# Optimization experiments

Measured on AMD Instinct MI355X. Metric: run time of the kernel, lower is better.

## Reference

```python
import jax, jax.numpy as jnp
import numpy as np

O, NI, F, D, NN, M = 2048, 16, 4, 128, 8, 8  # outfits, item slots, factors, dim, neighbors, valid slots
D2 = D // 2

def lrelu(x):
    return jax.nn.leaky_relu(x, 0.01)

def mlp2(x, W1, b1, W2, b2):
    # Linear -> LeakyReLU -> Linear -> LeakyReLU (Dropout is identity at inference)
    return lrelu(lrelu(x @ W1 + b1) @ W2 + b2)

def setup_inputs():
    ks = jax.random.split(jax.random.key(0), 16)
    s = 0.05
    pos = jnp.arange(NI)[None, :]
    outfit_items = jnp.where(pos < M, jax.random.randint(ks[0], (O, NI), 0, NI), -1)
    items_neighbor = jax.random.randint(ks[1], (O, NI, NN), -1, NI)
    items_feature = jax.random.normal(ks[2], (O, NI, D), dtype=jnp.float32)
    items_factors = jnp.zeros((O, NI, F, D), dtype=jnp.float32)
    p = {
        'cf_W1': jax.random.normal(ks[3], (F, D, D2)) * s,
        'cf_b1': jnp.zeros((F, D2)),
        'cf_W2': jax.random.normal(ks[4], (F, D2, D)) * s,
        'cf_b2': jnp.zeros((F, D)),
        'f2f_W1': jax.random.normal(ks[5], (D, D)) * s, 'f2f_b1': jnp.zeros((D,)),
        'f2f_W2': jax.random.normal(ks[6], (D, D)) * s, 'f2f_b2': jnp.zeros((D,)),
        'f2i_W1': jax.random.normal(ks[7], (D, D)) * s, 'f2i_b1': jnp.zeros((D,)),
        'f2i_W2': jax.random.normal(ks[8], (D, D)) * s, 'f2i_b2': jnp.zeros((D,)),
        'i2i_W1': jax.random.normal(ks[9], (D, D)) * s, 'i2i_b1': jnp.zeros((D,)),
        'i2i_W2': jax.random.normal(ks[10], (D, D)) * s, 'i2i_b2': jnp.zeros((D,)),
        'o2s_W': jax.random.normal(ks[11], (D, 1)) * s, 'o2s_b': jnp.zeros((1,)),
    }
    return dict(outfit_items=outfit_items, items_feature=items_feature,
                items_neighbor=items_neighbor, items_factors=items_factors, **p)

def _forward(outfit_items, items_feature, items_neighbor, items_factors,
             cf_W1, cf_b1, cf_W2, cf_b2, f2f_W1, f2f_b1, f2f_W2, f2f_b2,
             f2i_W1, f2i_b1, f2i_W2, f2i_b2, i2i_W1, i2i_b1, i2i_W2, i2i_b2,
             o2s_W, o2s_b):
    del items_factors  # creat_factors overwrites every entry in the original
    # --- creat_factors: per-factor 2-layer MLP on every item feature -> [O,NI,F,D]
    h = lrelu(jnp.einsum('oid,fde->oife', items_feature, cf_W1) + cf_b1)
    fac = lrelu(jnp.einsum('oife,fed->oifd', h, cf_W2) + cf_b2)

    # --- inter_factors: sequential over outfit slots; later slots read updated factors
    def outfit_fac(fac_o, oi_o, nbr_o):
        def step(f, i):
            valid = i != -1
            ic = jnp.maximum(i, 0)
            cand = jnp.concatenate([oi_o, nbr_o[ic]])                # [NI+NN]
            cm = (cand != -1) & (cand != i) & valid
            t = f[ic]                                                # [F,D] snapshot
            msg = mlp2(t[None] * f[jnp.maximum(cand, 0)],
                       f2f_W1, f2f_b1, f2f_W2, f2f_b2)               # [NI+NN,F,D]
            add = jnp.sum(jnp.where(cm[:, None, None], msg, 0.0), axis=0)
            return f.at[ic].add(jnp.where(valid, add, 0.0)), None
        f, _ = jax.lax.scan(step, fac_o, oi_o)
        return f
    fac = jax.vmap(outfit_fac)(fac, outfit_items, items_neighbor)

    # --- infer_items: feature[i] += sum_j f2i(fac[i,j]) for outfit members
    g = mlp2(fac, f2i_W1, f2i_b1, f2i_W2, f2i_b2).sum(axis=2)        # [O,NI,D]
    ic = jnp.maximum(outfit_items, 0)
    w = (outfit_items != -1).astype(g.dtype)                          # [O,NI]
    gsel = jnp.take_along_axis(g, ic[..., None], axis=1)
    scat = jax.vmap(lambda gs, idx, ww: jnp.zeros((NI, D), gs.dtype).at[idx].add(ww[:, None] * gs))
    feat = items_feature + scat(gsel, ic, w)

    # --- inter_items: sequential; current value detached (.data in original)
    def outfit_feat(fo_init, oi_o):
        jc = jnp.maximum(oi_o, 0)
        def step(fo, i):
            valid = i != -1
            ic_ = jnp.maximum(i, 0)
            t = jax.lax.stop_gradient(fo[ic_])
            msgs = mlp2(fo[jc], i2i_W1, i2i_b1, i2i_W2, i2i_b2)      # [NI,D]
            m = ((oi_o != -1) & (oi_o != i)).astype(fo.dtype)
            new = t + jnp.sum(m[:, None] * msgs, axis=0)
            return jnp.where(valid, fo.at[ic_].set(new), fo), None
        fo, _ = jax.lax.scan(step, fo_init, oi_o)
        return fo
    feat = jax.vmap(outfit_feat)(feat, outfit_items)

    # --- infer_outfit + score
    fsel = jnp.take_along_axis(feat, ic[..., None], axis=1)
    outfits = jnp.sum(w[..., None] * fsel, axis=1)                    # [O,D]
    scores = jax.nn.sigmoid(outfits @ o2s_W + o2s_b)[:, 0]            # [O]

    # --- com_loss: ||F F^T - I||_F^2 over valid slots (positional mask), / n_outfits
    G = jnp.einsum('oifd,oigd->oifg', fac, fac) - jnp.eye(F, dtype=fac.dtype)
    com = jnp.sum(w * jnp.sum(G * G, axis=(-1, -2))) / O
    return scores, jnp.reshape(com, (1,))

def reference(outfit_items, items_feature, items_neighbor, items_factors,
              cf_W1, cf_b1, cf_W2, cf_b2, f2f_W1, f2f_b1, f2f_W2, f2f_b2,
              f2i_W1, f2i_b1, f2i_W2, f2i_b2, i2i_W1, i2i_b1, i2i_W2, i2i_b2,
              o2s_W, o2s_b):
    return _forward(outfit_items, items_feature, items_neighbor, items_factors,
                    cf_W1, cf_b1, cf_W2, cf_b2, f2f_W1, f2f_b1, f2f_W2, f2f_b2,
                    f2i_W1, f2i_b1, f2i_W2, f2i_b2, i2i_W1, i2i_b1, i2i_W2, i2i_b2,
                    o2s_W, o2s_b)
```

## Files before the change

kernel.cpp:

```cpp
#include <hip/hip_runtime.h>
#include <hip/hip_bf16.h>
#include <math.h>


typedef __attribute__((ext_vector_type(8))) short short8;
typedef __attribute__((ext_vector_type(4))) float f32x4;

#define MFMA16(a, b, c) __builtin_amdgcn_mfma_f32_16x16x32_bf16(a, b, c, 0, 0, 0)

__device__ __forceinline__ float lrelu(float x) { return fmaxf(x, 0.01f * x); }

__device__ __forceinline__ ushort f2bf(float f) {
  unsigned u = __builtin_bit_cast(unsigned, f);
  u += 0x7fffu + ((u >> 16) & 1u);
  return (ushort)(u >> 16);
}
__device__ __forceinline__ float bflo(unsigned u) {
  return __builtin_bit_cast(float, u << 16);
}
__device__ __forceinline__ unsigned pk2(float a, float b) {
  float2 t; t.x = a; t.y = b;
  __hip_bfloat162 h = __float22bfloat162_rn(t);
  unsigned u;
  __builtin_memcpy(&u, &h, 4);
  return u;
}


__global__ __launch_bounds__(256) void prep_weights(
    const float* __restrict__ cfW1, const float* __restrict__ cfW2,
    const float* __restrict__ f2fW1, const float* __restrict__ f2fW2,
    const float* __restrict__ f2iW1, const float* __restrict__ f2iW2,
    const float* __restrict__ i2iW1, const float* __restrict__ i2iW2,
    ushort* __restrict__ ws, float* __restrict__ out) {
  const int idx = (int)(blockIdx.x * 256 + threadIdx.x);
  if (idx == 0) out[2048] = 0.0f;
  float v;
  if (idx < 32768) {
    int f = idx >> 13, r = idx & 8191, n = r >> 7, k = r & 127;
    v = cfW1[f * 8192 + k * 64 + n];
  } else if (idx < 65536) {
    int t = idx - 32768;
    int f = t >> 13, r = t & 8191, n = r >> 6, k = r & 63;
    v = cfW2[f * 8192 + k * 128 + n];
  } else {
    int t = idx - 65536;
    int seg = t >> 14, r = t & 16383, n = r >> 7, k = r & 127;
    const float* W = (seg == 0) ? f2fW1 : (seg == 1) ? f2fW2 :
                     (seg == 2) ? f2iW1 : (seg == 3) ? f2iW2 :
                     (seg == 4) ? i2iW1 : i2iW2;
    v = W[k * 128 + n];
  }
  ws[idx] = f2bf(v);
}

__global__ __launch_bounds__(512, 2) void mfgn_kernel(
    const int* __restrict__ outfit_items,
    const float* __restrict__ items_feature,
    const int* __restrict__ items_neighbor,
    const float* __restrict__ cfb1, const float* __restrict__ cfb2,
    const float* __restrict__ f2fb1, const float* __restrict__ f2fb2,
    const float* __restrict__ f2ib1, const float* __restrict__ f2ib2,
    const float* __restrict__ i2ib1, const float* __restrict__ i2ib2,
    const float* __restrict__ o2sW, const float* __restrict__ o2sb,
    const ushort* __restrict__ wsW,
    float* __restrict__ out)
{
  __shared__ float facL[16 * 528];
  __shared__ ushort prodS[64 * 136] __attribute__((aligned(16)));
  __shared__ ushort hidS[64 * 136] __attribute__((aligned(16)));
  __shared__ ushort featB[16 * 136] __attribute__((aligned(16)));
  __shared__ float redE[8];
  __shared__ int oiL[16];
  __shared__ int clAll[256];
  __shared__ int ncAll[16];
  __shared__ int vslL[16];
  __shared__ int refcntL[16];
  __shared__ int nvsL;

  const int o = blockIdx.x;
  const int tid = (int)threadIdx.x;
  const int lane = tid & 63;
  const int wid = tid >> 6;
  const int n16 = lane & 15;
  const int q = lane >> 4;
  const int kb = q * 8;
  const int col = wid * 16 + n16;
  const int fS = lane & 3, ciS = lane >> 2;
  const int kc0 = wid * 16;

  if (tid < 16) oiL[tid] = outfit_items[o * 16 + tid];
  {
    const int n = tid >> 5, d0 = (tid & 31) * 4;
    float4 v = *(const float4*)(items_feature + o * 2048 + tid * 4);
    uint2 pk; pk.x = pk2(v.x, v.y); pk.y = pk2(v.z, v.w);
    *(uint2*)(featB + n * 136 + d0) = pk;
  }
  if (tid == 0) {
    int cnt = 0;
    for (int s = 0; s < 16; ++s) refcntL[s] = 0;
    for (int s = 0; s < 16; ++s) {
      int v = oiL[s];
      if (v != -1) { vslL[cnt++] = s; refcntL[v]++; }
    }
    nvsL = cnt;
  }
  for (int s = wid; s < 16; s += 8) {
    const int iv = outfit_items[o * 16 + s];
    if (iv == -1) { if (lane == 0) ncAll[s] = 0; continue; }
    int cand = -1;
    if (lane < 24) cand = (lane < 16) ? outfit_items[o * 16 + lane]
                                      : items_neighbor[o * 128 + iv * 8 + (lane - 16)];
    bool ok = (lane < 24) && (cand != -1) && (cand != iv);
    unsigned long long bm = __ballot(ok);
    if (ok) clAll[s * 16 + __popcll(bm & ((1ull << lane) - 1ull))] = cand;
    if (lane == 0) ncAll[s] = (int)__popcll(bm);
  }
  __syncthreads();
  const int nvs = nvsL;

  {
    const int f = wid & 3, half = wid >> 2;
    short8 wA[2][4];
#pragma unroll
    for (int etl = 0; etl < 2; ++etl)
#pragma unroll
      for (int kt = 0; kt < 4; ++kt)
        wA[etl][kt] = *(const short8*)(wsW + (f * 64 + (half * 2 + etl) * 16 + n16) * 128
                                       + kt * 32 + kb);
    f32x4 acc[2];
#pragma unroll
    for (int etl = 0; etl < 2; ++etl)
      acc[etl] = *(const f32x4*)(cfb1 + f * 64 + (half * 2 + etl) * 16 + q * 4);
    for (int kt = 0; kt < 4; ++kt) {
      short8 x = *(const short8*)(featB + n16 * 136 + kt * 32 + kb);
      acc[0] = MFMA16(wA[0][kt], x, acc[0]);
      acc[1] = MFMA16(wA[1][kt], x, acc[1]);
    }
#pragma unroll
    for (int etl = 0; etl < 2; ++etl) {
      float h0 = lrelu(acc[etl][0]), h1 = lrelu(acc[etl][1]);
      float h2 = lrelu(acc[etl][2]), h3 = lrelu(acc[etl][3]);
      uint2 pk; pk.x = pk2(h0, h1); pk.y = pk2(h2, h3);
      *(uint2*)(hidS + (f * 16 + n16) * 136 + (half * 2 + etl) * 16 + q * 4) = pk;
    }
    __syncthreads();
    short8 wB[4][2];
#pragma unroll
    for (int ctl = 0; ctl < 4; ++ctl)
#pragma unroll
      for (int kt = 0; kt < 2; ++kt)
        wB[ctl][kt] = *(const short8*)(wsW + 32768 + (f * 128 + half * 64 + ctl * 16 + n16) * 64
                                       + kt * 32 + kb);
    f32x4 acc2[4];
#pragma unroll
    for (int ctl = 0; ctl < 4; ++ctl) {
      float b2 = cfb2[f * 128 + half * 64 + ctl * 16 + n16];
      acc2[ctl] = (f32x4){b2, b2, b2, b2};
    }
    for (int kt = 0; kt < 2; ++kt) {
      short8 h = *(const short8*)(hidS + (f * 16 + n16) * 136 + kt * 32 + kb);
#pragma unroll
      for (int ctl = 0; ctl < 4; ++ctl) acc2[ctl] = MFMA16(h, wB[ctl][kt], acc2[ctl]);
    }
#pragma unroll
    for (int ctl = 0; ctl < 4; ++ctl) {
      int c = half * 64 + ctl * 16 + n16;
#pragma unroll
      for (int r = 0; r < 4; ++r)
        facL[(q * 4 + r) * 528 + f * 132 + c] = lrelu(acc2[ctl][r]);
    }
    __syncthreads();
  }

  {
    short8 w1f[4], w2f[4];
#pragma unroll
    for (int kt = 0; kt < 4; ++kt) {
      w1f[kt] = *(const short8*)(wsW + 65536 + col * 128 + kt * 32 + kb);
      w2f[kt] = *(const short8*)(wsW + 81920 + col * 128 + kt * 32 + kb);
    }
    const f32x4 b1q = *(const f32x4*)(f2fb1 + wid * 16 + q * 4);
    const float b2v = f2fb2[col];

    auto stageB = [&](int s, int iv_, int nc_) {
      if (ciS < nc_) {
        const int cit = clAll[s * 16 + ciS];
        const float* tp = facL + iv_ * 528 + fS * 132 + kc0;
        const float* cp = facL + cit * 528 + fS * 132 + kc0;
#pragma unroll
        for (int i2 = 0; i2 < 2; ++i2) {
          float4 a0 = *(const float4*)(tp + i2 * 8), a1 = *(const float4*)(tp + i2 * 8 + 4);
          float4 c0 = *(const float4*)(cp + i2 * 8), c1 = *(const float4*)(cp + i2 * 8 + 4);
          uint4 u4;
          u4.x = pk2(a0.x * c0.x, a0.y * c0.y); u4.y = pk2(a0.z * c0.z, a0.w * c0.w);
          u4.z = pk2(a1.x * c1.x, a1.y * c1.y); u4.w = pk2(a1.z * c1.z, a1.w * c1.w);
          *(uint4*)(prodS + lane * 136 + kc0 + i2 * 8) = u4;
        }
      }
    };
    auto stageC = [&]() {
      const float* sp = facL + ciS * 528 + fS * 132 + kc0;
#pragma unroll
      for (int i2 = 0; i2 < 2; ++i2) {
        float4 a0 = *(const float4*)(sp + i2 * 8), a1 = *(const float4*)(sp + i2 * 8 + 4);
        uint4 u4;
        u4.x = pk2(a0.x, a0.y); u4.y = pk2(a0.z, a0.w);
        u4.z = pk2(a1.x, a1.y); u4.w = pk2(a1.z, a1.w);
        *(uint4*)(prodS + lane * 136 + kc0 + i2 * 8) = u4;
      }
    };

    if (nvs > 0) { const int s0 = vslL[0]; stageB(s0, oiL[s0], ncAll[s0]); }
    __syncthreads();

    for (int u = 0; u < nvs; ++u) {
      const int s = vslL[u];
      const int iv = oiL[s];
      const int nc = ncAll[s];
      f32x4 acc[4];
#pragma unroll
      for (int mt = 0; mt < 4; ++mt) acc[mt] = b1q;
      for (int kt = 0; kt < 4; ++kt)
#pragma unroll
        for (int mt = 0; mt < 4; ++mt) {
          short8 x = *(const short8*)(prodS + (mt * 16 + n16) * 136 + kt * 32 + kb);
          acc[mt] = MFMA16(w1f[kt], x, acc[mt]);
        }
#pragma unroll
      for (int mt = 0; mt < 4; ++mt) {
        float h0 = lrelu(acc[mt][0]), h1 = lrelu(acc[mt][1]);
        float h2 = lrelu(acc[mt][2]), h3 = lrelu(acc[mt][3]);
        uint2 pk; pk.x = pk2(h0, h1); pk.y = pk2(h2, h3);
        *(uint2*)(hidS + (mt * 16 + n16) * 136 + wid * 16 + q * 4) = pk;
      }
      __syncthreads();
      f32x4 acc2[4];
#pragma unroll
      for (int mt = 0; mt < 4; ++mt) acc2[mt] = (f32x4){b2v, b2v, b2v, b2v};
      for (int kt = 0; kt < 4; ++kt)
#pragma unroll
        for (int mt = 0; mt < 4; ++mt) {
          short8 h = *(const short8*)(hidS + (mt * 16 + n16) * 136 + kt * 32 + kb);
          acc2[mt] = MFMA16(h, w2f[kt], acc2[mt]);
        }
      float part[4] = {0.f, 0.f, 0.f, 0.f};
#pragma unroll
      for (int mt = 0; mt < 4; ++mt) {
        bool act = (mt * 4 + q) < nc;
        if (act) {
#pragma unroll
          for (int r = 0; r < 4; ++r) part[r] += lrelu(acc2[mt][r]);
        }
      }
#pragma unroll
      for (int r = 0; r < 4; ++r) {
        float v = part[r];
        v += __shfl_xor(v, 16);
        v += __shfl_xor(v, 32);
        part[r] = v;
      }
      if (q == 0) {
#pragma unroll
        for (int r = 0; r < 4; ++r)
          facL[iv * 528 + r * 132 + col] += part[r];
      }
      if (u + 1 < nvs) {
        const int s2 = vslL[u + 1];
        stageB(s2, oiL[s2], ncAll[s2]);
      } else {
        stageC();
      }
      __syncthreads();
    }
    if (nvs == 0) { stageC(); __syncthreads(); }
  }

  {
    short8 w1f[4], w2f[4];
#pragma unroll
    for (int kt = 0; kt < 4; ++kt) {
      w1f[kt] = *(const short8*)(wsW + 98304 + col * 128 + kt * 32 + kb);
      w2f[kt] = *(const short8*)(wsW + 114688 + col * 128 + kt * 32 + kb);
    }
    const f32x4 b1q = *(const f32x4*)(f2ib1 + wid * 16 + q * 4);
    const float b2v = f2ib2[col];
    f32x4 acc[4];
#pragma unroll
    for (int mt = 0; mt < 4; ++mt) acc[mt] = b1q;
    for (int kt = 0; kt < 4; ++kt)
#pragma unroll
      for (int mt = 0; mt < 4; ++mt) {
        short8 x = *(const short8*)(prodS + (mt * 16 + n16) * 136 + kt * 32 + kb);
        acc[mt] = MFMA16(w1f[kt], x, acc[mt]);
      }
#pragma unroll
    for (int mt = 0; mt < 4; ++mt) {
      float h0 = lrelu(acc[mt][0]), h1 = lrelu(acc[mt][1]);
      float h2 = lrelu(acc[mt][2]), h3 = lrelu(acc[mt][3]);
      uint2 pk; pk.x = pk2(h0, h1); pk.y = pk2(h2, h3);
      *(uint2*)(hidS + (mt * 16 + n16) * 136 + wid * 16 + q * 4) = pk;
    }
    __syncthreads();
    f32x4 acc2[4];
#pragma unroll
    for (int mt = 0; mt < 4; ++mt) acc2[mt] = (f32x4){b2v, b2v, b2v, b2v};
    for (int kt = 0; kt < 4; ++kt)
#pragma unroll
      for (int mt = 0; mt < 4; ++mt) {
        short8 h = *(const short8*)(hidS + (mt * 16 + n16) * 136 + kt * 32 + kb);
        acc2[mt] = MFMA16(h, w2f[kt], acc2[mt]);
      }
#pragma unroll
    for (int mt = 0; mt < 4; ++mt) {
      int item = mt * 4 + q;
      float g = 0.f;
#pragma unroll
      for (int r = 0; r < 4; ++r) g += lrelu(acc2[mt][r]);
      int a = item * 136 + col;
      featB[a] = f2bf(bflo((unsigned)featB[a]) + (float)refcntL[item] * g);
    }
    __syncthreads();
  }

  {
    short8 w1f[4], w2f[4];
#pragma unroll
    for (int kt = 0; kt < 4; ++kt) {
      w1f[kt] = *(const short8*)(wsW + 131072 + col * 128 + kt * 32 + kb);
      w2f[kt] = *(const short8*)(wsW + 147456 + col * 128 + kt * 32 + kb);
    }
    const f32x4 b1q = *(const f32x4*)(i2ib1 + wid * 16 + q * 4);
    const float b2v = i2ib2[col];
    short8 xc[4];
#pragma unroll
    for (int kt = 0; kt < 4; ++kt)
      xc[kt] = *(const short8*)(featB + n16 * 136 + kt * 32 + kb);

    for (int u = 0; u < nvs; ++u) {
      const int iv = oiL[vslL[u]];
      f32x4 acc = b1q;
      for (int kt = 0; kt < 4; ++kt) acc = MFMA16(w1f[kt], xc[kt], acc);
      {
        float h0 = lrelu(acc[0]), h1 = lrelu(acc[1]);
        float h2 = lrelu(acc[2]), h3 = lrelu(acc[3]);
        uint2 pk; pk.x = pk2(h0, h1); pk.y = pk2(h2, h3);
        *(uint2*)(hidS + n16 * 136 + wid * 16 + q * 4) = pk;
      }
      __syncthreads();
      f32x4 acc2 = (f32x4){b2v, b2v, b2v, b2v};
      for (int kt = 0; kt < 4; ++kt) {
        short8 h = *(const short8*)(hidS + n16 * 136 + kt * 32 + kb);
        acc2 = MFMA16(h, w2f[kt], acc2);
      }
      float part = 0.f;
#pragma unroll
      for (int r = 0; r < 4; ++r) {
        int item = q * 4 + r;
        float w = (item == iv) ? 0.0f : (float)refcntL[item];
        part += w * lrelu(acc2[r]);
      }
      part += __shfl_xor(part, 16);
      part += __shfl_xor(part, 32);
      if (q == 0) {
        int a = iv * 136 + col;
        featB[a] = f2bf(bflo((unsigned)featB[a]) + part);
      }
      __syncthreads();
      if (n16 == iv) {
#pragma unroll
        for (int kt = 0; kt < 4; ++kt)
          xc[kt] = *(const short8*)(featB + n16 * 136 + kt * 32 + kb);
      }
    }
  }

  if (tid < 128) {
    float sum = 0.0f;
    for (int u = 0; u < nvs; ++u)
      sum += bflo((unsigned)featB[oiL[vslL[u]] * 136 + tid]);
    float v = sum * o2sW[tid];
#pragma unroll
    for (int off = 1; off < 64; off <<= 1) v += __shfl_xor(v, off);
    if (lane == 0) redE[wid] = v;
  }
  __syncthreads();
  if (tid == 0) {
    float t = redE[0] + redE[1] + o2sb[0];
    out[o] = 1.0f / (1.0f + expf(-t));
  }

  {
    const int n = tid >> 5, f = (tid >> 3) & 3, g = (tid >> 1) & 3, h = tid & 1;
    float dot = 0.0f;
    if (f <= g) {
      const float* pa = facL + n * 528 + f * 132 + h * 64;
      const float* pb = facL + n * 528 + g * 132 + h * 64;
      for (int i = 0; i < 16; ++i) {
        float4 a = *(const float4*)(pa + i * 4);
        float4 b = *(const float4*)(pb + i * 4);
        dot += a.x * b.x + a.y * b.y + a.z * b.z + a.w * b.w;
      }
    }
    dot += __shfl_xor(dot, 1);
    float v = dot - ((f == g) ? 1.0f : 0.0f);
    float wgt = (f == g) ? 1.0f : 2.0f;
    float sq = (h == 0 && f <= g && oiL[n] != -1) ? wgt * v * v : 0.0f;
#pragma unroll
    for (int off = 1; off < 64; off <<= 1) sq += __shfl_xor(sq, off);
    __syncthreads();
    if (lane == 0) redE[wid] = sq;
    __syncthreads();
    if (tid == 0) {
      float tot = 0.f;
#pragma unroll
      for (int w = 0; w < 8; ++w) tot += redE[w];
      atomicAdd(out + 2048, tot * (1.0f / 2048.0f));
    }
  }
}

extern "C" void kernel_launch(void* const* d_in, const int* in_sizes, int n_in,
                              void* d_out, int out_size, void* d_ws, size_t ws_size,
                              hipStream_t stream) {
  float* out = (float*)d_out;
  ushort* ws = (ushort*)d_ws;
  hipLaunchKernelGGL(prep_weights, dim3(640), dim3(256), 0, stream,
                     (const float*)d_in[4], (const float*)d_in[6],
                     (const float*)d_in[8], (const float*)d_in[10],
                     (const float*)d_in[12], (const float*)d_in[14],
                     (const float*)d_in[16], (const float*)d_in[18],
                     ws, out);
  hipLaunchKernelGGL(mfgn_kernel, dim3(2048), dim3(512), 0, stream,
                     (const int*)d_in[0],
                     (const float*)d_in[1],
                     (const int*)d_in[2],
                     (const float*)d_in[5], (const float*)d_in[7],
                     (const float*)d_in[9], (const float*)d_in[11],
                     (const float*)d_in[13], (const float*)d_in[15],
                     (const float*)d_in[17], (const float*)d_in[19],
                     (const float*)d_in[20], (const float*)d_in[21],
                     (const ushort*)ws,
                     out);
}
```

Before: 336.5 us.

## Store MFMA operand tiles in lane-contiguous fragment layout in shared memory

Replaces the padded row-major (stride 136) shared-memory layouts of prodS, hidS and featB with a fragment-ordered layout. Each MFMA B-operand read becomes a contiguous lane*8 short8 load at a tile base, and writers compute swizzled addresses instead. This aims to cut LDS bank conflicts and address arithmetic in the inner MFMA loops, at the cost of more complex and scattered store and element-access indexing.

```diff
diff --git a/kernel.cpp b/kernel.cpp
--- a/kernel.cpp
+++ b/kernel.cpp
@@ -67,9 +67,9 @@
     float* __restrict__ out)
 {
   __shared__ float facL[16 * 528];
-  __shared__ ushort prodS[64 * 136] __attribute__((aligned(16)));
-  __shared__ ushort hidS[64 * 136] __attribute__((aligned(16)));
-  __shared__ ushort featB[16 * 136] __attribute__((aligned(16)));
+  __shared__ ushort prodS[8192] __attribute__((aligned(16)));
+  __shared__ ushort hidS[8192] __attribute__((aligned(16)));
+  __shared__ ushort featB[2048] __attribute__((aligned(16)));
   __shared__ float redE[8];
   __shared__ int oiL[16];
   __shared__ int clAll[256];
@@ -86,15 +86,20 @@
   const int q = lane >> 4;
   const int kb = q * 8;
   const int col = wid * 16 + n16;
+  const int lx = lane * 8;
   const int fS = lane & 3, ciS = lane >> 2;
   const int kc0 = wid * 16;
+  const int q0 = (wid & 1) * 2;
+  const int sWA = ((wid >> 1) * 4 + (lane >> 4)) * 512 + (lane & 15) * 8;
+  const int hwB = (wid >> 1) * 2048 + ((wid & 1) * 2 + (q >> 1)) * 128 + n16 * 8 + (q & 1) * 4;
+  const int fbCol = (col >> 5) * 512 + ((col >> 3) & 3) * 128 + (col & 7);
 
   if (tid < 16) oiL[tid] = outfit_items[o * 16 + tid];
   {
     const int n = tid >> 5, d0 = (tid & 31) * 4;
     float4 v = *(const float4*)(items_feature + o * 2048 + tid * 4);
     uint2 pk; pk.x = pk2(v.x, v.y); pk.y = pk2(v.z, v.w);
-    *(uint2*)(featB + n * 136 + d0) = pk;
+    *(uint2*)(featB + (d0 >> 5) * 512 + (((d0 >> 3) & 3) * 16 + n) * 8 + (d0 & 7)) = pk;
   }
   if (tid == 0) {
     int cnt = 0;
@@ -133,7 +138,7 @@
     for (int etl = 0; etl < 2; ++etl)
       acc[etl] = *(const f32x4*)(cfb1 + f * 64 + (half * 2 + etl) * 16 + q * 4);
     for (int kt = 0; kt < 4; ++kt) {
-      short8 x = *(const short8*)(featB + n16 * 136 + kt * 32 + kb);
+      short8 x = *(const short8*)(featB + kt * 512 + lx);
       acc[0] = MFMA16(wA[0][kt], x, acc[0]);
       acc[1] = MFMA16(wA[1][kt], x, acc[1]);
     }
@@ -142,7 +147,8 @@
       float h0 = lrelu(acc[etl][0]), h1 = lrelu(acc[etl][1]);
       float h2 = lrelu(acc[etl][2]), h3 = lrelu(acc[etl][3]);
       uint2 pk; pk.x = pk2(h0, h1); pk.y = pk2(h2, h3);
-      *(uint2*)(hidS + (f * 16 + n16) * 136 + (half * 2 + etl) * 16 + q * 4) = pk;
+      *(uint2*)(hidS + half * 2048 + f * 512 + (etl * 2 + (q >> 1)) * 128
+                + n16 * 8 + (q & 1) * 4) = pk;
     }
     __syncthreads();
     short8 wB[4][2];
@@ -159,7 +165,7 @@
       acc2[ctl] = (f32x4){b2, b2, b2, b2};
     }
     for (int kt = 0; kt < 2; ++kt) {
-      short8 h = *(const short8*)(hidS + (f * 16 + n16) * 136 + kt * 32 + kb);
+      short8 h = *(const short8*)(hidS + (kt * 4 + f) * 512 + lx);
 #pragma unroll
       for (int ctl = 0; ctl < 4; ++ctl) acc2[ctl] = MFMA16(h, wB[ctl][kt], acc2[ctl]);
     }
@@ -189,25 +195,25 @@
         const float* tp = facL + iv_ * 528 + fS * 132 + kc0;
         const float* cp = facL + cit * 528 + fS * 132 + kc0;
 #pragma unroll
-        for (int i2 = 0; i2 < 2; ++i2) {
-          float4 a0 = *(const float4*)(tp + i2 * 8), a1 = *(const float4*)(tp + i2 * 8 + 4);
-          float4 c0 = *(const float4*)(cp + i2 * 8), c1 = *(const float4*)(cp + i2 * 8 + 4);
+        for (int g = 0; g < 2; ++g) {
+          float4 a0 = *(const float4*)(tp + g * 8), a1 = *(const float4*)(tp + g * 8 + 4);
+          float4 c0 = *(const float4*)(cp + g * 8), c1 = *(const float4*)(cp + g * 8 + 4);
           uint4 u4;
           u4.x = pk2(a0.x * c0.x, a0.y * c0.y); u4.y = pk2(a0.z * c0.z, a0.w * c0.w);
           u4.z = pk2(a1.x * c1.x, a1.y * c1.y); u4.w = pk2(a1.z * c1.z, a1.w * c1.w);
-          *(uint4*)(prodS + lane * 136 + kc0 + i2 * 8) = u4;
+          *(uint4*)(prodS + sWA + (q0 + g) * 128) = u4;
         }
       }
     };
     auto stageC = [&]() {
       const float* sp = facL + ciS * 528 + fS * 132 + kc0;
 #pragma unroll
-      for (int i2 = 0; i2 < 2; ++i2) {
-        float4 a0 = *(const float4*)(sp + i2 * 8), a1 = *(const float4*)(sp + i2 * 8 + 4);
+      for (int g = 0; g < 2; ++g) {
+        float4 a0 = *(const float4*)(sp + g * 8), a1 = *(const float4*)(sp + g * 8 + 4);
         uint4 u4;
         u4.x = pk2(a0.x, a0.y); u4.y = pk2(a0.z, a0.w);
         u4.z = pk2(a1.x, a1.y); u4.w = pk2(a1.z, a1.w);
-        *(uint4*)(prodS + lane * 136 + kc0 + i2 * 8) = u4;
+        *(uint4*)(prodS + sWA + (q0 + g) * 128) = u4;
       }
     };
 
@@ -224,7 +230,7 @@
       for (int kt = 0; kt < 4; ++kt)
 #pragma unroll
         for (int mt = 0; mt < 4; ++mt) {
-          short8 x = *(const short8*)(prodS + (mt * 16 + n16) * 136 + kt * 32 + kb);
+          short8 x = *(const short8*)(prodS + (kt * 4 + mt) * 512 + lx);
           acc[mt] = MFMA16(w1f[kt], x, acc[mt]);
         }
 #pragma unroll
@@ -232,7 +238,7 @@
         float h0 = lrelu(acc[mt][0]), h1 = lrelu(acc[mt][1]);
         float h2 = lrelu(acc[mt][2]), h3 = lrelu(acc[mt][3]);
         uint2 pk; pk.x = pk2(h0, h1); pk.y = pk2(h2, h3);
-        *(uint2*)(hidS + (mt * 16 + n16) * 136 + wid * 16 + q * 4) = pk;
+        *(uint2*)(hidS + hwB + mt * 512) = pk;
       }
       __syncthreads();
       f32x4 acc2[4];
@@ -241,7 +247,7 @@
       for (int kt = 0; kt < 4; ++kt)
 #pragma unroll
         for (int mt = 0; mt < 4; ++mt) {
-          short8 h = *(const short8*)(hidS + (mt * 16 + n16) * 136 + kt * 32 + kb);
+          short8 h = *(const short8*)(hidS + (kt * 4 + mt) * 512 + lx);
           acc2[mt] = MFMA16(h, w2f[kt], acc2[mt]);
         }
       float part[4] = {0.f, 0.f, 0.f, 0.f};
@@ -291,7 +297,7 @@
     for (int kt = 0; kt < 4; ++kt)
 #pragma unroll
       for (int mt = 0; mt < 4; ++mt) {
-        short8 x = *(const short8*)(prodS + (mt * 16 + n16) * 136 + kt * 32 + kb);
+        short8 x = *(const short8*)(prodS + (kt * 4 + mt) * 512 + lx);
         acc[mt] = MFMA16(w1f[kt], x, acc[mt]);
       }
 #pragma unroll
@@ -299,7 +305,7 @@
       float h0 = lrelu(acc[mt][0]), h1 = lrelu(acc[mt][1]);
       float h2 = lrelu(acc[mt][2]), h3 = lrelu(acc[mt][3]);
       uint2 pk; pk.x = pk2(h0, h1); pk.y = pk2(h2, h3);
-      *(uint2*)(hidS + (mt * 16 + n16) * 136 + wid * 16 + q * 4) = pk;
+      *(uint2*)(hidS + hwB + mt * 512) = pk;
     }
     __syncthreads();
     f32x4 acc2[4];
@@ -308,7 +314,7 @@
     for (int kt = 0; kt < 4; ++kt)
 #pragma unroll
       for (int mt = 0; mt < 4; ++mt) {
-        short8 h = *(const short8*)(hidS + (mt * 16 + n16) * 136 + kt * 32 + kb);
+        short8 h = *(const short8*)(hidS + (kt * 4 + mt) * 512 + lx);
         acc2[mt] = MFMA16(h, w2f[kt], acc2[mt]);
       }
 #pragma unroll
@@ -317,7 +323,7 @@
       float g = 0.f;
 #pragma unroll
       for (int r = 0; r < 4; ++r) g += lrelu(acc2[mt][r]);
-      int a = item * 136 + col;
+      int a = fbCol + item * 8;
       featB[a] = f2bf(bflo((unsigned)featB[a]) + (float)refcntL[item] * g);
     }
     __syncthreads();
@@ -335,7 +341,7 @@
     short8 xc[4];
 #pragma unroll
     for (int kt = 0; kt < 4; ++kt)
-      xc[kt] = *(const short8*)(featB + n16 * 136 + kt * 32 + kb);
+      xc[kt] = *(const short8*)(featB + kt * 512 + lx);
 
     for (int u = 0; u < nvs; ++u) {
       const int iv = oiL[vslL[u]];
@@ -345,12 +351,12 @@
         float h0 = lrelu(acc[0]), h1 = lrelu(acc[1]);
         float h2 = lrelu(acc[2]), h3 = lrelu(acc[3]);
         uint2 pk; pk.x = pk2(h0, h1); pk.y = pk2(h2, h3);
-        *(uint2*)(hidS + n16 * 136 + wid * 16 + q * 4) = pk;
+        *(uint2*)(hidS + hwB) = pk;
       }
       __syncthreads();
       f32x4 acc2 = (f32x4){b2v, b2v, b2v, b2v};
       for (int kt = 0; kt < 4; ++kt) {
-        short8 h = *(const short8*)(hidS + n16 * 136 + kt * 32 + kb);
+        short8 h = *(const short8*)(hidS + kt * 2048 + lx);
         acc2 = MFMA16(h, w2f[kt], acc2);
       }
       float part = 0.f;
@@ -363,22 +369,25 @@
       part += __shfl_xor(part, 16);
       part += __shfl_xor(part, 32);
       if (q == 0) {
-        int a = iv * 136 + col;
+        int a = fbCol + iv * 8;
         featB[a] = f2bf(bflo((unsigned)featB[a]) + part);
       }
       __syncthreads();
       if (n16 == iv) {
 #pragma unroll
         for (int kt = 0; kt < 4; ++kt)
-          xc[kt] = *(const short8*)(featB + n16 * 136 + kt * 32 + kb);
+          xc[kt] = *(const short8*)(featB + kt * 512 + lx);
       }
     }
   }
 
   if (tid < 128) {
+    const int eb = (tid >> 5) * 512 + ((tid >> 3) & 3) * 128 + (tid & 7);
     float sum = 0.0f;
-    for (int u = 0; u < nvs; ++u)
-      sum += bflo((unsigned)featB[oiL[vslL[u]] * 136 + tid]);
+    for (int u = 0; u < nvs; ++u) {
+      int it = oiL[vslL[u]];
+      sum += bflo((unsigned)featB[eb + it * 8]);
+    }
     float v = sum * o2sW[tid];
 #pragma unroll
     for (int off = 1; off < 64; off <<= 1) v += __shfl_xor(v, off);
```

Result: faster. 320.9 us (-4.6%).
